# Performance work log

Hardware: AMD Instinct MI355X
Metric: run time of the kernel (lower is better)

## Reference

```python
import jax, jax.numpy as jnp
import numpy as np

B, Q, K, D = 16, 2048, 2048, 512

def setup_inputs() -> dict:
    key = jax.random.key(0)
    k1, k2, k3 = jax.random.split(key, 3)
    query = jax.random.normal(k1, (B, Q, D), dtype=jnp.float32)
    values = jax.random.normal(k2, (B, K, D), dtype=jnp.float32)
    # nn.Linear(D, D, bias=False) weight, applied as values @ W.T
    W_attn = jax.random.normal(k3, (D, D), dtype=jnp.float32) * (1.0 / np.sqrt(D))
    return {"query": query, "values": values, "W_attn": W_attn}

def reference(query, values, W_attn):
    # keys = Linear(values) = values @ W_attn.T  -> [B, K, D]
    keys = jnp.einsum('bkd,ed->bke', values, W_attn)
    # scores[b,q,k] = query[b,q,:] . keys[b,k,:]
    scores = jnp.einsum('bqd,bkd->bqk', query, keys)
    attention_weights = jax.nn.softmax(scores, axis=-1)
    context = jnp.einsum('bqk,bkd->bqd', attention_weights, values)
    return (context, attention_weights)
```

## Files before the change

### kernel.cpp

```cpp
#include <hip/hip_runtime.h>
#include <hip/hip_bf16.h>


#define B_ 16
#define Q_ 2048
#define K_ 2048
#define D_ 512

typedef _Float16 half8  __attribute__((ext_vector_type(8)));
typedef _Float16 half4v __attribute__((ext_vector_type(4)));
typedef float    floatx4 __attribute__((ext_vector_type(4)));

__device__ __forceinline__ void gld16(const _Float16* g, _Float16* l) {
  __builtin_amdgcn_global_load_lds(
      (const __attribute__((address_space(1))) void*)g,
      (__attribute__((address_space(3))) void*)l, 16, 0, 0);
}

template <bool OUT_HALF>
__global__ __launch_bounds__(256, 2)
void gemm_bt_f16(const _Float16* __restrict__ A, const _Float16* __restrict__ Bm,
                 void* __restrict__ Cv, int M, int N, int Kd,
                 long sA, long sB, long sC)
{
  const int b  = blockIdx.z;
  const _Float16* Ab = A + (long)b * sA;
  const _Float16* Bb = Bm + (long)b * sB;
  const int m0 = blockIdx.y * 128, n0 = blockIdx.x * 128;

  __shared__ _Float16 As[128 * 32];
  __shared__ _Float16 Bs[128 * 32];

  const int tid = threadIdx.x, wave = tid >> 6, lane = tid & 63;
  const int wm = wave >> 1, wn = wave & 1;
  floatx4 acc[4][4] = {};

  const int srow = wave * 16 + (lane >> 2);
  const int skof = (lane & 3) * 8;
  _Float16* la0 = As + wave * 512 + lane * 8;
  _Float16* la1 = la0 + 2048;
  _Float16* lb0 = Bs + wave * 512 + lane * 8;
  _Float16* lb1 = lb0 + 2048;
  const _Float16* ga = Ab + (long)(m0 + srow) * Kd + skof;
  const _Float16* gb = Bb + (long)(n0 + srow) * Kd + skof;

  const int fr = lane & 15, fk = (lane >> 4) * 8;

  for (int k0 = 0; k0 < Kd; k0 += 32) {
    gld16(ga + k0, la0);
    gld16(ga + 64l * Kd + k0, la1);
    gld16(gb + k0, lb0);
    gld16(gb + 64l * Kd + k0, lb1);
    __syncthreads();

    half8 af[4], bf[4];
#pragma unroll
    for (int t = 0; t < 4; t++) {
      af[t] = *(const half8*)(As + (wm * 64 + t * 16 + fr) * 32 + fk);
      bf[t] = *(const half8*)(Bs + (wn * 64 + t * 16 + fr) * 32 + fk);
    }
#pragma unroll
    for (int mt = 0; mt < 4; mt++)
#pragma unroll
      for (int nt = 0; nt < 4; nt++)
        acc[mt][nt] = __builtin_amdgcn_mfma_f32_16x16x32_f16(af[mt], bf[nt], acc[mt][nt], 0, 0, 0);
    __syncthreads();
  }

  const int orow = (lane >> 4) * 4, ocol = lane & 15;
  if constexpr (OUT_HALF) {
    _Float16* Cp = (_Float16*)Cv + (long)b * sC;
#pragma unroll
    for (int mt = 0; mt < 4; mt++)
#pragma unroll
      for (int nt = 0; nt < 4; nt++)
#pragma unroll
        for (int r = 0; r < 4; r++)
          Cp[(long)(m0 + wm * 64 + mt * 16 + orow + r) * N + (n0 + wn * 64 + nt * 16 + ocol)] =
              (_Float16)acc[mt][nt][r];
  } else {
    float* Cp = (float*)Cv + (long)b * sC;
#pragma unroll
    for (int mt = 0; mt < 4; mt++)
#pragma unroll
      for (int nt = 0; nt < 4; nt++)
#pragma unroll
        for (int r = 0; r < 4; r++)
          Cp[(long)(m0 + wm * 64 + mt * 16 + orow + r) * N + (n0 + wn * 64 + nt * 16 + ocol)] =
              acc[mt][nt][r];
  }
}

template <bool OUT_HALF>
__global__ __launch_bounds__(256, 2)
void gemm_a32_bt(const float* __restrict__ A, const _Float16* __restrict__ Bm,
                 void* __restrict__ Cv, int M, int N, int Kd, int lda,
                 long sA, long sB, long sC)
{
  const int b  = blockIdx.z;
  const float*    Ab = A + (long)b * sA;
  const _Float16* Bb = Bm + (long)b * sB;
  const int m0 = blockIdx.y * 128, n0 = blockIdx.x * 128;

  __shared__ _Float16 As[128 * 32];
  __shared__ _Float16 Bs[128 * 32];

  const int tid = threadIdx.x, wave = tid >> 6, lane = tid & 63;
  const int wm = wave >> 1, wn = wave & 1;
  floatx4 acc[4][4] = {};

  const int srow = wave * 16 + (lane >> 2);
  const int skof = (lane & 3) * 8;
  _Float16* lb0 = Bs + wave * 512 + lane * 8;
  _Float16* lb1 = lb0 + 2048;
  const _Float16* gb = Bb + (long)(n0 + srow) * Kd + skof;

  const int arow = tid >> 1, akc = (tid & 1) * 16;
  const float* ga = Ab + (long)(m0 + arow) * lda + akc;

  const int fr = lane & 15, fk = (lane >> 4) * 8;

  for (int k0 = 0; k0 < Kd; k0 += 32) {
    gld16(gb + k0, lb0);
    gld16(gb + 64l * Kd + k0, lb1);

    const float* ap = ga + k0;
    float4 f0 = *(const float4*)(ap);
    float4 f1 = *(const float4*)(ap + 4);
    float4 f2 = *(const float4*)(ap + 8);
    float4 f3 = *(const float4*)(ap + 12);
    half8 h0, h1;
    h0[0] = (_Float16)f0.x; h0[1] = (_Float16)f0.y; h0[2] = (_Float16)f0.z; h0[3] = (_Float16)f0.w;
    h0[4] = (_Float16)f1.x; h0[5] = (_Float16)f1.y; h0[6] = (_Float16)f1.z; h0[7] = (_Float16)f1.w;
    h1[0] = (_Float16)f2.x; h1[1] = (_Float16)f2.y; h1[2] = (_Float16)f2.z; h1[3] = (_Float16)f2.w;
    h1[4] = (_Float16)f3.x; h1[5] = (_Float16)f3.y; h1[6] = (_Float16)f3.z; h1[7] = (_Float16)f3.w;
    *(half8*)(As + arow * 32 + akc)     = h0;
    *(half8*)(As + arow * 32 + akc + 8) = h1;

    __syncthreads();

    half8 af[4], bf[4];
#pragma unroll
    for (int t = 0; t < 4; t++) {
      af[t] = *(const half8*)(As + (wm * 64 + t * 16 + fr) * 32 + fk);
      bf[t] = *(const half8*)(Bs + (wn * 64 + t * 16 + fr) * 32 + fk);
    }
#pragma unroll
    for (int mt = 0; mt < 4; mt++)
#pragma unroll
      for (int nt = 0; nt < 4; nt++)
        acc[mt][nt] = __builtin_amdgcn_mfma_f32_16x16x32_f16(af[mt], bf[nt], acc[mt][nt], 0, 0, 0);
    __syncthreads();
  }

  const int orow = (lane >> 4) * 4, ocol = lane & 15;
  if constexpr (OUT_HALF) {
    _Float16* Cp = (_Float16*)Cv + (long)b * sC;
#pragma unroll
    for (int mt = 0; mt < 4; mt++)
#pragma unroll
      for (int nt = 0; nt < 4; nt++)
#pragma unroll
        for (int r = 0; r < 4; r++)
          Cp[(long)(m0 + wm * 64 + mt * 16 + orow + r) * N + (n0 + wn * 64 + nt * 16 + ocol)] =
              (_Float16)acc[mt][nt][r];
  } else {
    float* Cp = (float*)Cv + (long)b * sC;
#pragma unroll
    for (int mt = 0; mt < 4; mt++)
#pragma unroll
      for (int nt = 0; nt < 4; nt++)
#pragma unroll
        for (int r = 0; r < 4; r++)
          Cp[(long)(m0 + wm * 64 + mt * 16 + orow + r) * N + (n0 + wn * 64 + nt * 16 + ocol)] =
              acc[mt][nt][r];
  }
}

template <bool EMIT_H>
__global__ __launch_bounds__(256)
void softmax_rows(float* __restrict__ S, _Float16* __restrict__ P)
{
  float* p = S + (long)blockIdx.x * 2048;
  const int tid = threadIdx.x, lane = tid & 63, wave = tid >> 6;

  float4 v0 = *(const float4*)(p + tid * 4);
  float4 v1 = *(const float4*)(p + 1024 + tid * 4);

  float mx = fmaxf(fmaxf(fmaxf(v0.x, v0.y), fmaxf(v0.z, v0.w)),
                   fmaxf(fmaxf(v1.x, v1.y), fmaxf(v1.z, v1.w)));
#pragma unroll
  for (int off = 32; off; off >>= 1) mx = fmaxf(mx, __shfl_down(mx, off, 64));

  __shared__ float red[8];
  if (lane == 0) red[wave] = mx;
  __syncthreads();
  mx = fmaxf(fmaxf(red[0], red[1]), fmaxf(red[2], red[3]));

  v0.x = __expf(v0.x - mx); v0.y = __expf(v0.y - mx);
  v0.z = __expf(v0.z - mx); v0.w = __expf(v0.w - mx);
  v1.x = __expf(v1.x - mx); v1.y = __expf(v1.y - mx);
  v1.z = __expf(v1.z - mx); v1.w = __expf(v1.w - mx);

  float s = v0.x + v0.y + v0.z + v0.w + v1.x + v1.y + v1.z + v1.w;
#pragma unroll
  for (int off = 32; off; off >>= 1) s += __shfl_down(s, off, 64);
  if (lane == 0) red[4 + wave] = s;
  __syncthreads();
  s = red[4] + red[5] + red[6] + red[7];

  float inv = 1.0f / s;
  v0.x *= inv; v0.y *= inv; v0.z *= inv; v0.w *= inv;
  v1.x *= inv; v1.y *= inv; v1.z *= inv; v1.w *= inv;
  *(float4*)(p + tid * 4) = v0;
  *(float4*)(p + 1024 + tid * 4) = v1;

  if constexpr (EMIT_H) {
    _Float16* ph = P + (long)blockIdx.x * 2048;
    half4v h0, h1;
    h0[0] = (_Float16)v0.x; h0[1] = (_Float16)v0.y;
    h0[2] = (_Float16)v0.z; h0[3] = (_Float16)v0.w;
    h1[0] = (_Float16)v1.x; h1[1] = (_Float16)v1.y;
    h1[2] = (_Float16)v1.z; h1[3] = (_Float16)v1.w;
    *(half4v*)(ph + tid * 4) = h0;
    *(half4v*)(ph + 1024 + tid * 4) = h1;
  }
}

__global__ __launch_bounds__(256)
void convert_q(const float4* __restrict__ q, half4v* __restrict__ qh)
{
  long i = (long)blockIdx.x * 256 + threadIdx.x;
  float4 a = q[i];
  half4v h;
  h[0] = (_Float16)a.x; h[1] = (_Float16)a.y; h[2] = (_Float16)a.z; h[3] = (_Float16)a.w;
  qh[i] = h;
}

__global__ __launch_bounds__(256)
void transpose_v(const float* __restrict__ v, _Float16* __restrict__ vt)
{
  __shared__ float tile[32][33];
  const int b = blockIdx.z, kk = blockIdx.y * 32, ee = blockIdx.x * 32;
  const float* vp = v + (long)b * K_ * D_;
  _Float16* vtp = vt + (long)b * D_ * K_;
  const int tx = threadIdx.x & 31, ty = threadIdx.x >> 5;
#pragma unroll
  for (int i = 0; i < 32; i += 8)
    tile[ty + i][tx] = vp[(long)(kk + ty + i) * D_ + ee + tx];
  __syncthreads();
#pragma unroll
  for (int i = 0; i < 32; i += 8)
    vtp[(long)(ee + ty + i) * K_ + kk + tx] = (_Float16)tile[tx][ty + i];
}

extern "C" void kernel_launch(void* const* d_in, const int* in_sizes, int n_in,
                              void* d_out, int out_size, void* d_ws, size_t ws_size,
                              hipStream_t stream)
{
  const float* q = (const float*)d_in[0];
  const float* v = (const float*)d_in[1];
  const float* w = (const float*)d_in[2];

  float* ctx    = (float*)d_out;
  float* scores = ctx + (long)B_ * Q_ * D_;

  const long nQD = (long)B_ * Q_ * D_;
  const long nKD = (long)B_ * K_ * D_;
  const long nDK = (long)B_ * D_ * K_;
  const long nQK = (long)B_ * Q_ * K_;

  const size_t need_fast = (size_t)(512 * 512 + nDK + nQK) * sizeof(_Float16);
  const bool fast = ws_size >= need_fast;

  _Float16 *wh, *vth, *qh, *kh, *ph;
  if (fast) {
    wh  = (_Float16*)d_ws;
    vth = wh + 512 * 512;
    ph  = vth + nDK;
    qh  = ph;
    kh  = qh + nQD;
  } else {
    qh  = (_Float16*)d_ws;
    kh  = qh + nQD;
    vth = kh + nKD;
    wh  = vth + nDK;
    ph  = nullptr;
  }

  convert_q<<<16384, 256, 0, stream>>>((const float4*)q, (half4v*)qh);
  convert_q<<<256,   256, 0, stream>>>((const float4*)w, (half4v*)wh);
  transpose_v<<<dim3(D_ / 32, K_ / 32, B_), 256, 0, stream>>>(v, vth);

  gemm_a32_bt<true><<<dim3(D_ / 128, K_ / 128, B_), 256, 0, stream>>>(
      v, wh, kh, K_, D_, D_, D_, (long)K_ * D_, 0l, (long)K_ * D_);

  gemm_bt_f16<false><<<dim3(K_ / 128, Q_ / 128, B_), 256, 0, stream>>>(
      qh, kh, scores, Q_, K_, D_, (long)Q_ * D_, (long)K_ * D_, (long)Q_ * K_);

  if (fast)
    softmax_rows<true><<<B_ * Q_, 256, 0, stream>>>(scores, ph);
  else
    softmax_rows<false><<<B_ * Q_, 256, 0, stream>>>(scores, nullptr);

  if (fast)
    gemm_bt_f16<false><<<dim3(D_ / 128, Q_ / 128, B_), 256, 0, stream>>>(
        ph, vth, ctx, Q_, D_, K_, (long)Q_ * K_, (long)D_ * K_, (long)Q_ * D_);
  else
    gemm_a32_bt<false><<<dim3(D_ / 128, Q_ / 128, B_), 256, 0, stream>>>(
        scores, vth, ctx, Q_, D_, K_, K_, (long)Q_ * K_, (long)D_ * K_, (long)Q_ * D_);
}
```

Baseline: 785.1 us.

## Replace GEMMs with 256x256 double-buffered swizzled MFMA kernel with ping-pong scheduling

Replaces the 128x128 single-buffered GEMM kernels with one 256x256-tile, 512-thread kernel. It double-buffers LDS, swizzles LDS columns to avoid bank conflicts, and interleaves global-to-LDS staging with MFMA quadrants using barriers and s_setprio. The key projection now reads an fp16 copy of values, produced inside the transpose kernel, instead of converting fp32 on the fly. The fallback path for small workspaces is dropped, so the code now assumes a larger workspace. The 256-wide tiles also cut the number of blocks for the D=512-wide outputs.

```diff
diff --git a/kernel.cpp b/kernel.cpp
--- a/kernel.cpp
+++ b/kernel.cpp
@@ -1,5 +1,4 @@
 #include <hip/hip_runtime.h>
-#include <hip/hip_bf16.h>
 
 
 #define B_ 16
@@ -17,167 +16,139 @@
       (__attribute__((address_space(3))) void*)l, 16, 0, 0);
 }
 
+
+#define STAGE_A(DBUF, T, H)                                                    \
+  { gld16(Ab + (long)(m0 + (H)*128 +      srow) * Kd + (T)*64 + scolsw,        \
+          &As[DBUF][(H)*8192 +        wave*512]);                              \
+    gld16(Ab + (long)(m0 + (H)*128 + 64 + srow) * Kd + (T)*64 + scolsw,        \
+          &As[DBUF][(H)*8192 + 4096 + wave*512]); }
+
+#define STAGE_B(DBUF, T, H)                                                    \
+  { gld16(Bb + (long)(n0 + (H)*128 +      srow) * Kd + (T)*64 + scolsw,        \
+          &Bs[DBUF][(H)*8192 +        wave*512]);                              \
+    gld16(Bb + (long)(n0 + (H)*128 + 64 + srow) * Kd + (T)*64 + scolsw,        \
+          &Bs[DBUF][(H)*8192 + 4096 + wave*512]); }
+
+#define RD_A(DST, BUF, MH)                                                     \
+  _Pragma("unroll") for (int mi = 0; mi < 4; ++mi)                             \
+  _Pragma("unroll") for (int ks = 0; ks < 2; ++ks)                             \
+    DST[mi][ks] = *(const half8*)(                                             \
+        &As[BUF][(wm*128 + ((MH)*4 + mi)*16 + fr)*64 + ks*32 + fksw]);
+
+#define RD_B(DST, BUF, NH)                                                     \
+  _Pragma("unroll") for (int ni = 0; ni < 2; ++ni)                             \
+  _Pragma("unroll") for (int ks = 0; ks < 2; ++ks)                             \
+    DST[ni][ks] = *(const half8*)(                                             \
+        &Bs[BUF][(wn*64 + ((NH)*2 + ni)*16 + fr)*64 + ks*32 + fksw]);
+
+#define QUAD(AARR, BARR, MH, NH)                                               \
+  _Pragma("unroll") for (int mi = 0; mi < 4; ++mi)                             \
+  _Pragma("unroll") for (int ni = 0; ni < 2; ++ni)                             \
+  _Pragma("unroll") for (int ks = 0; ks < 2; ++ks)                             \
+    acc[(MH)*4 + mi][(NH)*2 + ni] = __builtin_amdgcn_mfma_f32_16x16x32_f16(    \
+        AARR[mi][ks], BARR[ni][ks], acc[(MH)*4 + mi][(NH)*2 + ni], 0, 0, 0);
+
+#define BAR_MID()                                                              \
+  __builtin_amdgcn_s_barrier();                                                \
+  asm volatile("s_waitcnt lgkmcnt(0)" ::: "memory");                           \
+  __builtin_amdgcn_s_setprio(1);
+
+#define BAR_END()                                                              \
+  __builtin_amdgcn_s_setprio(0);                                               \
+  __builtin_amdgcn_s_barrier();
+
 template <bool OUT_HALF>
-__global__ __launch_bounds__(256, 2)
-void gemm_bt_f16(const _Float16* __restrict__ A, const _Float16* __restrict__ Bm,
-                 void* __restrict__ Cv, int M, int N, int Kd,
-                 long sA, long sB, long sC)
-{
-  const int b  = blockIdx.z;
+__global__ __launch_bounds__(512, 2)
+void gemm256(const _Float16* __restrict__ A, const _Float16* __restrict__ Bm,
+             void* __restrict__ Cv, int M, int N, int Kd,
+             long sA, long sB, long sC)
+{
+  __shared__ _Float16 As[2][16384];
+  __shared__ _Float16 Bs[2][16384];
+
+  const int b = blockIdx.z;
   const _Float16* Ab = A + (long)b * sA;
   const _Float16* Bb = Bm + (long)b * sB;
-  const int m0 = blockIdx.y * 128, n0 = blockIdx.x * 128;
-
-  __shared__ _Float16 As[128 * 32];
-  __shared__ _Float16 Bs[128 * 32];
+  const int m0 = blockIdx.y * 256, n0 = blockIdx.x * 256;
+  (void)M;
 
   const int tid = threadIdx.x, wave = tid >> 6, lane = tid & 63;
-  const int wm = wave >> 1, wn = wave & 1;
-  floatx4 acc[4][4] = {};
-
-  const int srow = wave * 16 + (lane >> 2);
-  const int skof = (lane & 3) * 8;
-  _Float16* la0 = As + wave * 512 + lane * 8;
-  _Float16* la1 = la0 + 2048;
-  _Float16* lb0 = Bs + wave * 512 + lane * 8;
-  _Float16* lb1 = lb0 + 2048;
-  const _Float16* ga = Ab + (long)(m0 + srow) * Kd + skof;
-  const _Float16* gb = Bb + (long)(n0 + srow) * Kd + skof;
-
-  const int fr = lane & 15, fk = (lane >> 4) * 8;
-
-  for (int k0 = 0; k0 < Kd; k0 += 32) {
-    gld16(ga + k0, la0);
-    gld16(ga + 64l * Kd + k0, la1);
-    gld16(gb + k0, lb0);
-    gld16(gb + 64l * Kd + k0, lb1);
-    __syncthreads();
-
-    half8 af[4], bf[4];
-#pragma unroll
-    for (int t = 0; t < 4; t++) {
-      af[t] = *(const half8*)(As + (wm * 64 + t * 16 + fr) * 32 + fk);
-      bf[t] = *(const half8*)(Bs + (wn * 64 + t * 16 + fr) * 32 + fk);
-    }
-#pragma unroll
-    for (int mt = 0; mt < 4; mt++)
-#pragma unroll
-      for (int nt = 0; nt < 4; nt++)
-        acc[mt][nt] = __builtin_amdgcn_mfma_f32_16x16x32_f16(af[mt], bf[nt], acc[mt][nt], 0, 0, 0);
-    __syncthreads();
+  const int wm = wave >> 2, wn = wave & 3;
+
+  const int srow = tid >> 3;
+  const int scolsw = ((tid & 7) * 8) ^ (((tid >> 5) & 1) << 4);
+  const int fr = lane & 15;
+  const int fksw = ((lane >> 4) * 8) ^ (((fr >> 2) & 1) << 4);
+
+  floatx4 acc[8][4] = {};
+
+  STAGE_A(0, 0, 0) STAGE_A(0, 0, 1) STAGE_B(0, 0, 0) STAGE_B(0, 0, 1)
+  STAGE_A(1, 1, 0) STAGE_A(1, 1, 1)
+  asm volatile("s_waitcnt vmcnt(4)" ::: "memory");
+  __builtin_amdgcn_s_barrier();
+
+  const int NI = Kd >> 7;
+  for (int j = 0; j < NI; ++j) {
+    const int E = 2 * j, O = E + 1;
+    const bool ns = (j + 1 < NI);
+    half8 aL[4][2], aH[4][2], bL[2][2], bH[2][2];
+
+    RD_A(aL, 0, 0) RD_B(bL, 0, 0)
+    STAGE_B(1, O, 0)
+    BAR_MID() QUAD(aL, bL, 0, 0) BAR_END()
+
+    RD_A(aH, 0, 1) RD_B(bH, 0, 1)
+    STAGE_B(1, O, 1)
+    BAR_MID() QUAD(aL, bH, 0, 1) BAR_END()
+
+    if (ns) STAGE_A(0, E + 2, 0)
+    BAR_MID() QUAD(aH, bH, 1, 1) BAR_END()
+
+    if (ns) { STAGE_A(0, E + 2, 1)
+              asm volatile("s_waitcnt vmcnt(4)" ::: "memory"); }
+    else    { asm volatile("s_waitcnt vmcnt(0)" ::: "memory"); }
+    BAR_MID() QUAD(aH, bL, 1, 0) BAR_END()
+
+    RD_A(aL, 1, 0) RD_B(bL, 1, 0)
+    if (ns) STAGE_B(0, E + 2, 0)
+    BAR_MID() QUAD(aL, bL, 0, 0) BAR_END()
+
+    RD_A(aH, 1, 1) RD_B(bH, 1, 1)
+    if (ns) STAGE_B(0, E + 2, 1)
+    BAR_MID() QUAD(aL, bH, 0, 1) BAR_END()
+
+    if (ns) STAGE_A(1, O + 2, 0)
+    BAR_MID() QUAD(aH, bH, 1, 1) BAR_END()
+
+    if (ns) { STAGE_A(1, O + 2, 1)
+              asm volatile("s_waitcnt vmcnt(4)" ::: "memory"); }
+    BAR_MID() QUAD(aH, bL, 1, 0) BAR_END()
   }
 
   const int orow = (lane >> 4) * 4, ocol = lane & 15;
   if constexpr (OUT_HALF) {
     _Float16* Cp = (_Float16*)Cv + (long)b * sC;
 #pragma unroll
-    for (int mt = 0; mt < 4; mt++)
-#pragma unroll
-      for (int nt = 0; nt < 4; nt++)
-#pragma unroll
-        for (int r = 0; r < 4; r++)
-          Cp[(long)(m0 + wm * 64 + mt * 16 + orow + r) * N + (n0 + wn * 64 + nt * 16 + ocol)] =
+    for (int mt = 0; mt < 8; ++mt)
+#pragma unroll
+      for (int nt = 0; nt < 4; ++nt)
+#pragma unroll
+        for (int r = 0; r < 4; ++r)
+          Cp[(long)(m0 + wm*128 + mt*16 + orow + r) * N + (n0 + wn*64 + nt*16 + ocol)] =
               (_Float16)acc[mt][nt][r];
   } else {
     float* Cp = (float*)Cv + (long)b * sC;
 #pragma unroll
-    for (int mt = 0; mt < 4; mt++)
-#pragma unroll
-      for (int nt = 0; nt < 4; nt++)
-#pragma unroll
-        for (int r = 0; r < 4; r++)
-          Cp[(long)(m0 + wm * 64 + mt * 16 + orow + r) * N + (n0 + wn * 64 + nt * 16 + ocol)] =
+    for (int mt = 0; mt < 8; ++mt)
+#pragma unroll
+      for (int nt = 0; nt < 4; ++nt)
+#pragma unroll
+        for (int r = 0; r < 4; ++r)
+          Cp[(long)(m0 + wm*128 + mt*16 + orow + r) * N + (n0 + wn*64 + nt*16 + ocol)] =
               acc[mt][nt][r];
   }
 }
 
-template <bool OUT_HALF>
-__global__ __launch_bounds__(256, 2)
-void gemm_a32_bt(const float* __restrict__ A, const _Float16* __restrict__ Bm,
-                 void* __restrict__ Cv, int M, int N, int Kd, int lda,
-                 long sA, long sB, long sC)
-{
-  const int b  = blockIdx.z;
-  const float*    Ab = A + (long)b * sA;
-  const _Float16* Bb = Bm + (long)b * sB;
-  const int m0 = blockIdx.y * 128, n0 = blockIdx.x * 128;
-
-  __shared__ _Float16 As[128 * 32];
-  __shared__ _Float16 Bs[128 * 32];
-
-  const int tid = threadIdx.x, wave = tid >> 6, lane = tid & 63;
-  const int wm = wave >> 1, wn = wave & 1;
-  floatx4 acc[4][4] = {};
-
-  const int srow = wave * 16 + (lane >> 2);
-  const int skof = (lane & 3) * 8;
-  _Float16* lb0 = Bs + wave * 512 + lane * 8;
-  _Float16* lb1 = lb0 + 2048;
-  const _Float16* gb = Bb + (long)(n0 + srow) * Kd + skof;
-
-  const int arow = tid >> 1, akc = (tid & 1) * 16;
-  const float* ga = Ab + (long)(m0 + arow) * lda + akc;
-
-  const int fr = lane & 15, fk = (lane >> 4) * 8;
-
-  for (int k0 = 0; k0 < Kd; k0 += 32) {
-    gld16(gb + k0, lb0);
-    gld16(gb + 64l * Kd + k0, lb1);
-
-    const float* ap = ga + k0;
-    float4 f0 = *(const float4*)(ap);
-    float4 f1 = *(const float4*)(ap + 4);
-    float4 f2 = *(const float4*)(ap + 8);
-    float4 f3 = *(const float4*)(ap + 12);
-    half8 h0, h1;
-    h0[0] = (_Float16)f0.x; h0[1] = (_Float16)f0.y; h0[2] = (_Float16)f0.z; h0[3] = (_Float16)f0.w;
-    h0[4] = (_Float16)f1.x; h0[5] = (_Float16)f1.y; h0[6] = (_Float16)f1.z; h0[7] = (_Float16)f1.w;
-    h1[0] = (_Float16)f2.x; h1[1] = (_Float16)f2.y; h1[2] = (_Float16)f2.z; h1[3] = (_Float16)f2.w;
-    h1[4] = (_Float16)f3.x; h1[5] = (_Float16)f3.y; h1[6] = (_Float16)f3.z; h1[7] = (_Float16)f3.w;
-    *(half8*)(As + arow * 32 + akc)     = h0;
-    *(half8*)(As + arow * 32 + akc + 8) = h1;
-
-    __syncthreads();
-
-    half8 af[4], bf[4];
-#pragma unroll
-    for (int t = 0; t < 4; t++) {
-      af[t] = *(const half8*)(As + (wm * 64 + t * 16 + fr) * 32 + fk);
-      bf[t] = *(const half8*)(Bs + (wn * 64 + t * 16 + fr) * 32 + fk);
-    }
-#pragma unroll
-    for (int mt = 0; mt < 4; mt++)
-#pragma unroll
-      for (int nt = 0; nt < 4; nt++)
-        acc[mt][nt] = __builtin_amdgcn_mfma_f32_16x16x32_f16(af[mt], bf[nt], acc[mt][nt], 0, 0, 0);
-    __syncthreads();
-  }
-
-  const int orow = (lane >> 4) * 4, ocol = lane & 15;
-  if constexpr (OUT_HALF) {
-    _Float16* Cp = (_Float16*)Cv + (long)b * sC;
-#pragma unroll
-    for (int mt = 0; mt < 4; mt++)
-#pragma unroll
-      for (int nt = 0; nt < 4; nt++)
-#pragma unroll
-        for (int r = 0; r < 4; r++)
-          Cp[(long)(m0 + wm * 64 + mt * 16 + orow + r) * N + (n0 + wn * 64 + nt * 16 + ocol)] =
-              (_Float16)acc[mt][nt][r];
-  } else {
-    float* Cp = (float*)Cv + (long)b * sC;
-#pragma unroll
-    for (int mt = 0; mt < 4; mt++)
-#pragma unroll
-      for (int nt = 0; nt < 4; nt++)
-#pragma unroll
-        for (int r = 0; r < 4; r++)
-          Cp[(long)(m0 + wm * 64 + mt * 16 + orow + r) * N + (n0 + wn * 64 + nt * 16 + ocol)] =
-              acc[mt][nt][r];
-  }
-}
-
-template <bool EMIT_H>
 __global__ __launch_bounds__(256)
 void softmax_rows(float* __restrict__ S, _Float16* __restrict__ P)
 {
@@ -215,16 +186,14 @@
   *(float4*)(p + tid * 4) = v0;
   *(float4*)(p + 1024 + tid * 4) = v1;
 
-  if constexpr (EMIT_H) {
-    _Float16* ph = P + (long)blockIdx.x * 2048;
-    half4v h0, h1;
-    h0[0] = (_Float16)v0.x; h0[1] = (_Float16)v0.y;
-    h0[2] = (_Float16)v0.z; h0[3] = (_Float16)v0.w;
-    h1[0] = (_Float16)v1.x; h1[1] = (_Float16)v1.y;
-    h1[2] = (_Float16)v1.z; h1[3] = (_Float16)v1.w;
-    *(half4v*)(ph + tid * 4) = h0;
-    *(half4v*)(ph + 1024 + tid * 4) = h1;
-  }
+  _Float16* ph = P + (long)blockIdx.x * 2048;
+  half4v h0, h1;
+  h0[0] = (_Float16)v0.x; h0[1] = (_Float16)v0.y;
+  h0[2] = (_Float16)v0.z; h0[3] = (_Float16)v0.w;
+  h1[0] = (_Float16)v1.x; h1[1] = (_Float16)v1.y;
+  h1[2] = (_Float16)v1.z; h1[3] = (_Float16)v1.w;
+  *(half4v*)(ph + tid * 4) = h0;
+  *(half4v*)(ph + 1024 + tid * 4) = h1;
 }
 
 __global__ __launch_bounds__(256)
@@ -238,16 +207,21 @@
 }
 
 __global__ __launch_bounds__(256)
-void transpose_v(const float* __restrict__ v, _Float16* __restrict__ vt)
+void transpose_v(const float* __restrict__ v, _Float16* __restrict__ vt,
+                 _Float16* __restrict__ vh)
 {
   __shared__ float tile[32][33];
   const int b = blockIdx.z, kk = blockIdx.y * 32, ee = blockIdx.x * 32;
   const float* vp = v + (long)b * K_ * D_;
   _Float16* vtp = vt + (long)b * D_ * K_;
+  _Float16* vhp = vh + (long)b * K_ * D_;
   const int tx = threadIdx.x & 31, ty = threadIdx.x >> 5;
 #pragma unroll
-  for (int i = 0; i < 32; i += 8)
-    tile[ty + i][tx] = vp[(long)(kk + ty + i) * D_ + ee + tx];
+  for (int i = 0; i < 32; i += 8) {
+    float x = vp[(long)(kk + ty + i) * D_ + ee + tx];
+    tile[ty + i][tx] = x;
+    vhp[(long)(kk + ty + i) * D_ + ee + tx] = (_Float16)x;
+  }
   __syncthreads();
 #pragma unroll
   for (int i = 0; i < 32; i += 8)
@@ -270,43 +244,26 @@
   const long nDK = (long)B_ * D_ * K_;
   const long nQK = (long)B_ * Q_ * K_;
 
-  const size_t need_fast = (size_t)(512 * 512 + nDK + nQK) * sizeof(_Float16);
-  const bool fast = ws_size >= need_fast;
-
-  _Float16 *wh, *vth, *qh, *kh, *ph;
-  if (fast) {
-    wh  = (_Float16*)d_ws;
-    vth = wh + 512 * 512;
-    ph  = vth + nDK;
-    qh  = ph;
-    kh  = qh + nQD;
-  } else {
-    qh  = (_Float16*)d_ws;
-    kh  = qh + nQD;
-    vth = kh + nKD;
-    wh  = vth + nDK;
-    ph  = nullptr;
-  }
+  _Float16* wh  = (_Float16*)d_ws;
+  _Float16* vth = wh + 512 * 512;
+  _Float16* ph  = vth + nDK;
+  _Float16* qh  = ph;
+  _Float16* kh  = qh + nQD;
+  _Float16* vh  = kh + nKD;
+  (void)ws_size;
 
   convert_q<<<16384, 256, 0, stream>>>((const float4*)q, (half4v*)qh);
   convert_q<<<256,   256, 0, stream>>>((const float4*)w, (half4v*)wh);
-  transpose_v<<<dim3(D_ / 32, K_ / 32, B_), 256, 0, stream>>>(v, vth);
-
-  gemm_a32_bt<true><<<dim3(D_ / 128, K_ / 128, B_), 256, 0, stream>>>(
-      v, wh, kh, K_, D_, D_, D_, (long)K_ * D_, 0l, (long)K_ * D_);
-
-  gemm_bt_f16<false><<<dim3(K_ / 128, Q_ / 128, B_), 256, 0, stream>>>(
+  transpose_v<<<dim3(D_ / 32, K_ / 32, B_), 256, 0, stream>>>(v, vth, vh);
+
+  gemm256<true><<<dim3(D_ / 256, K_ / 256, B_), 512, 0, stream>>>(
+      vh, wh, kh, K_, D_, D_, (long)K_ * D_, 0l, (long)K_ * D_);
+
+  gemm256<false><<<dim3(K_ / 256, Q_ / 256, B_), 512, 0, stream>>>(
       qh, kh, scores, Q_, K_, D_, (long)Q_ * D_, (long)K_ * D_, (long)Q_ * K_);
 
-  if (fast)
-    softmax_rows<true><<<B_ * Q_, 256, 0, stream>>>(scores, ph);
-  else
-    softmax_rows<false><<<B_ * Q_, 256, 0, stream>>>(scores, nullptr);
-
-  if (fast)
-    gemm_bt_f16<false><<<dim3(D_ / 128, Q_ / 128, B_), 256, 0, stream>>>(
-        ph, vth, ctx, Q_, D_, K_, (long)Q_ * K_, (long)D_ * K_, (long)Q_ * D_);
-  else
-    gemm_a32_bt<false><<<dim3(D_ / 128, Q_ / 128, B_), 256, 0, stream>>>(
-        scores, vth, ctx, Q_, D_, K_, K_, (long)Q_ * K_, (long)D_ * K_, (long)Q_ * D_);
-}
+  softmax_rows<<<B_ * Q_, 256, 0, stream>>>(scores, ph);
+
+  gemm256<false><<<dim3(D_ / 256, Q_ / 256, B_), 512, 0, stream>>>(
+      ph, vth, ctx, Q_, D_, K_, (long)Q_ * K_, (long)D_ * K_, (long)Q_ * D_);
+}
```

New measurement: 778.1 us. Within noise of the previous version (-0.9%).
